# Performance work log

Hardware: AMD Instinct MI355X
Metric: run time of the kernel (lower is better)

## Reference

```python
import jax, jax.numpy as jnp
import numpy as np

D_MODEL = 1024

def setup_inputs() -> dict:
    key = jax.random.key(0)
    ks = jax.random.split(key, 7)
    s = 1.0 / np.sqrt(D_MODEL)
    x = jax.random.normal(ks[0], (4, 2048, D_MODEL), dtype=jnp.float32)
    wq_w = jax.random.uniform(ks[1], (D_MODEL, D_MODEL), jnp.float32, -s, s)
    wq_b = jax.random.uniform(ks[2], (D_MODEL,), jnp.float32, -s, s)
    wk_w = jax.random.uniform(ks[3], (D_MODEL, D_MODEL), jnp.float32, -s, s)
    wk_b = jax.random.uniform(ks[4], (D_MODEL,), jnp.float32, -s, s)
    wv_w = jax.random.uniform(ks[5], (D_MODEL, D_MODEL), jnp.float32, -s, s)
    wv_b = jax.random.uniform(ks[6], (D_MODEL,), jnp.float32, -s, s)
    return {"x": x, "wq_w": wq_w, "wq_b": wq_b, "wk_w": wk_w, "wk_b": wk_b, "wv_w": wv_w, "wv_b": wv_b}

def reference(x, wq_w, wq_b, wk_w, wk_b, wv_w, wv_b):
    # Linear: x @ W^T + b (torch nn.Linear convention)
    q = jnp.einsum('bsd,ed->bse', x, wq_w) + wq_b
    k = jnp.einsum('bsd,ed->bse', x, wk_w) + wk_b
    v = jnp.einsum('bsd,ed->bse', x, wv_w) + wv_b
    scale = 1.0 / jnp.sqrt(jnp.asarray(k.shape[-1], dtype=q.dtype))
    logits = jnp.einsum('bqd,bkd->bqk', q, k) * scale  # [B, S, S]
    attn = jax.nn.softmax(logits, axis=-1)
    out = jnp.einsum('bqk,bkd->bqd', attn, v)
    return (attn, out)
```

## Files before the change

kernel.cpp:

```cpp
#include <hip/hip_runtime.h>

typedef unsigned short u16;
typedef u16 u16x4 __attribute__((ext_vector_type(4)));
typedef u16 u16x8 __attribute__((ext_vector_type(8)));
typedef __bf16 bf16x8 __attribute__((ext_vector_type(8)));
typedef float f32x16 __attribute__((ext_vector_type(16)));

static __device__ __forceinline__ u16 f2bf(float f) {
  unsigned u = __builtin_bit_cast(unsigned, f);
  u += 0x7fffu + ((u >> 16) & 1u);
  return (u16)(u >> 16);
}
static __device__ __forceinline__ float bf2f(u16 h) {
  return __builtin_bit_cast(float, ((unsigned)h) << 16);
}

static __device__ __forceinline__ void gload_lds16(const u16* g, u16* l) {
  u16* gn = const_cast<u16*>(g);
  __builtin_amdgcn_global_load_lds(
      (__attribute__((address_space(1))) unsigned int*)gn,
      (__attribute__((address_space(3))) unsigned int*)l,
      16, 0, 0);
}

__global__ __launch_bounds__(256)
void cvt_f32_bf16(const float* __restrict__ in, u16* __restrict__ out) {
  const int i = blockIdx.x * 256 + threadIdx.x;
  float4 f = ((const float4*)in)[i];
  u16x4 o = { f2bf(f.x), f2bf(f.y), f2bf(f.z), f2bf(f.w) };
  ((u16x4*)out)[i] = o;
}

__global__ __launch_bounds__(256)
void cvt_w3(const float* __restrict__ a, const float* __restrict__ b,
            const float* __restrict__ c, u16* __restrict__ out) {
  const int blk = blockIdx.x;
  const int w = blk >> 10;
  const float* src = (w == 0) ? a : (w == 1) ? b : c;
  const int i = (blk & 1023) * 256 + threadIdx.x;
  float4 f = ((const float4*)src)[i];
  u16x4 o = { f2bf(f.x), f2bf(f.y), f2bf(f.z), f2bf(f.w) };
  ((u16x4*)(out + (size_t)w * 1048576ULL))[i] = o;
}

template<int MODE>
__global__ __launch_bounds__(256)
void gemm_bt(const u16* __restrict__ Ain, const u16* __restrict__ Bin,
             void* __restrict__ Cv,
             const float* __restrict__ b0, const float* __restrict__ b1,
             const float* __restrict__ b2,
             int lda, int ldb, int ldc, int K,
             unsigned long long sA, unsigned long long sB, unsigned long long sC,
             int nbx, int nby)
{
  constexpr int BM = 128, BN = 128, BK = 64;
  __shared__ alignas(16) u16 As[BM * BK];
  __shared__ alignas(16) u16 Bs[BN * BK];

  const int nbxy = nbx * nby;
  const int bid  = blockIdx.x;
  const int flat = (bid & 7) * ((int)gridDim.x >> 3) + (bid >> 3);
  const int z    = flat / nbxy;
  const int rr   = flat - z * nbxy;
  const int width = nbx << 3;
  const int gid  = rr / width;
  const int rw   = rr - gid * width;
  const int by   = (gid << 3) + (rw & 7);
  const int bx   = rw >> 3;

  const u16* A = Ain + z * sA;
  const u16* B = Bin + z * sB;

  const int tid  = threadIdx.x;
  const int wave = tid >> 6;
  const int lane = tid & 63;
  const int l32  = lane & 31;
  const int half = lane >> 5;
  const int wr   = wave >> 1;
  const int wc   = wave & 1;

  const int m0 = by * BM;
  const int n0 = bx * BN;

  const int lr = lane >> 3;
  const int sc = ((lane & 7) ^ lr) * 8;
  const u16* Ag = A + (size_t)(m0 + wave * 32 + lr) * lda + sc;
  const u16* Bg = B + (size_t)(n0 + wave * 32 + lr) * ldb + sc;
  u16* Asb = &As[(wave * 32) * BK];
  u16* Bsb = &Bs[(wave * 32) * BK];

  f32x16 acc[2][2];
  #pragma unroll
  for (int i = 0; i < 2; ++i)
    #pragma unroll
    for (int j = 0; j < 2; ++j)
      #pragma unroll
      for (int r = 0; r < 16; ++r)
        acc[i][j][r] = 0.f;

  for (int k0 = 0; k0 < K; k0 += BK) {
    gload_lds16(Ag + k0,                    Asb);
    gload_lds16(Ag + (size_t) 8 * lda + k0, Asb +  8 * BK);
    gload_lds16(Ag + (size_t)16 * lda + k0, Asb + 16 * BK);
    gload_lds16(Ag + (size_t)24 * lda + k0, Asb + 24 * BK);
    gload_lds16(Bg + k0,                    Bsb);
    gload_lds16(Bg + (size_t) 8 * ldb + k0, Bsb +  8 * BK);
    gload_lds16(Bg + (size_t)16 * ldb + k0, Bsb + 16 * BK);
    gload_lds16(Bg + (size_t)24 * ldb + k0, Bsb + 24 * BK);
    __syncthreads();

    #pragma unroll
    for (int ks = 0; ks < 4; ++ks) {
      bf16x8 af[2], bfr[2];
      #pragma unroll
      for (int ti = 0; ti < 2; ++ti) {
        const int row = wr * 64 + ti * 32 + l32;
        const int ch  = ((ks * 2 + half) ^ (row & 7)) * 8;
        af[ti] = *(const bf16x8*)&As[row * BK + ch];
      }
      #pragma unroll
      for (int tj = 0; tj < 2; ++tj) {
        const int row = wc * 64 + tj * 32 + l32;
        const int ch  = ((ks * 2 + half) ^ (row & 7)) * 8;
        bfr[tj] = *(const bf16x8*)&Bs[row * BK + ch];
      }
      #pragma unroll
      for (int ti = 0; ti < 2; ++ti)
        #pragma unroll
        for (int tj = 0; tj < 2; ++tj)
          acc[ti][tj] = __builtin_amdgcn_mfma_f32_32x32x16_bf16(af[ti], bfr[tj], acc[ti][tj], 0, 0, 0);
    }
    __syncthreads();
  }

  const int colb = n0 + wc * 64 + l32;
  const int rowb = m0 + wr * 64 + 4 * half;

  if constexpr (MODE == 0) {
    const int g = n0 >> 10;
    u16* Qb = (u16*)Cv;
    if (g < 2) {
      u16* Cb = Qb + (size_t)g * 8388608ULL;
      const float* bp = (g == 0) ? b0 : b1;
      const float qs = (g == 0) ? 0.03125f : 1.0f;
      #pragma unroll
      for (int tj = 0; tj < 2; ++tj) {
        const int col = (colb + tj * 32) & 1023;
        const float bv = bp[col];
        #pragma unroll
        for (int ti = 0; ti < 2; ++ti)
          #pragma unroll
          for (int g4 = 0; g4 < 4; ++g4)
            #pragma unroll
            for (int r = 0; r < 4; ++r) {
              const int row = rowb + ti * 32 + g4 * 8 + r;
              Cb[(size_t)row * 1024 + col] = f2bf((acc[ti][tj][g4 * 4 + r] + bv) * qs);
            }
      }
    } else {
      u16* Vt = Qb + 16777216ULL;
      #pragma unroll
      for (int tj = 0; tj < 2; ++tj) {
        const int col = (colb + tj * 32) & 1023;
        const float bv = b2[col];
        #pragma unroll
        for (int ti = 0; ti < 2; ++ti)
          #pragma unroll
          for (int g4 = 0; g4 < 4; ++g4) {
            const int row = rowb + ti * 32 + g4 * 8;
            u16x4 o;
            #pragma unroll
            for (int r = 0; r < 4; ++r) o[r] = f2bf(acc[ti][tj][g4 * 4 + r] + bv);
            const size_t idx = ((size_t)((row >> 11) * 1024 + col)) * 2048 + (row & 2047);
            *(u16x4*)&Vt[idx] = o;
          }
      }
    }
  } else if constexpr (MODE == 2) {
    u16* Cb = (u16*)Cv + z * sC;
    #pragma unroll
    for (int tj = 0; tj < 2; ++tj) {
      const int col = colb + tj * 32;
      #pragma unroll
      for (int ti = 0; ti < 2; ++ti)
        #pragma unroll
        for (int g4 = 0; g4 < 4; ++g4)
          #pragma unroll
          for (int r = 0; r < 4; ++r) {
            const int row = rowb + ti * 32 + g4 * 8 + r;
            Cb[(size_t)row * ldc + col] = f2bf(acc[ti][tj][g4 * 4 + r]);
          }
    }
  } else {
    float* Cf = (float*)Cv + z * sC;
    #pragma unroll
    for (int tj = 0; tj < 2; ++tj) {
      const int col = colb + tj * 32;
      #pragma unroll
      for (int ti = 0; ti < 2; ++ti)
        #pragma unroll
        for (int g4 = 0; g4 < 4; ++g4)
          #pragma unroll
          for (int r = 0; r < 4; ++r) {
            const int row = rowb + ti * 32 + g4 * 8 + r;
            Cf[(size_t)row * ldc + col] = acc[ti][tj][g4 * 4 + r];
          }
    }
  }
}

__global__ __launch_bounds__(256)
void softmax_rows(u16* __restrict__ logits, float* __restrict__ attn) {
  const int row = blockIdx.x;
  const int tid = threadIdx.x;
  u16*   lp = logits + (size_t)row * 2048 + tid * 8;
  float* ap = attn   + (size_t)row * 2048 + tid * 8;

  u16x8 raw = *(const u16x8*)lp;
  float v[8];
  #pragma unroll
  for (int j = 0; j < 8; ++j) v[j] = bf2f(raw[j]);

  float mx = v[0];
  #pragma unroll
  for (int j = 1; j < 8; ++j) mx = fmaxf(mx, v[j]);
  #pragma unroll
  for (int o = 32; o > 0; o >>= 1) mx = fmaxf(mx, __shfl_xor(mx, o, 64));

  __shared__ float smax[4], ssum[4];
  const int wv = tid >> 6, ln = tid & 63;
  if (ln == 0) smax[wv] = mx;
  __syncthreads();
  mx = fmaxf(fmaxf(smax[0], smax[1]), fmaxf(smax[2], smax[3]));

  float s = 0.f;
  #pragma unroll
  for (int j = 0; j < 8; ++j) { v[j] = __expf(v[j] - mx); s += v[j]; }
  #pragma unroll
  for (int o = 32; o > 0; o >>= 1) s += __shfl_xor(s, o, 64);
  if (ln == 0) ssum[wv] = s;
  __syncthreads();
  s = (ssum[0] + ssum[1]) + (ssum[2] + ssum[3]);
  const float inv = 1.f / s;

  u16x8 ob;
  #pragma unroll
  for (int j = 0; j < 8; ++j) { v[j] *= inv; ob[j] = f2bf(v[j]); }
  float4* apv = (float4*)ap;
  apv[0] = make_float4(v[0], v[1], v[2], v[3]);
  apv[1] = make_float4(v[4], v[5], v[6], v[7]);
  *(u16x8*)lp = ob;
}

extern "C" void kernel_launch(void* const* d_in, const int* in_sizes, int n_in,
                              void* d_out, int out_size, void* d_ws, size_t ws_size,
                              hipStream_t stream) {
  (void)in_sizes; (void)n_in; (void)out_size; (void)ws_size;
  const float* x    = (const float*)d_in[0];
  const float* wq_w = (const float*)d_in[1];
  const float* wq_b = (const float*)d_in[2];
  const float* wk_w = (const float*)d_in[3];
  const float* wk_b = (const float*)d_in[4];
  const float* wv_w = (const float*)d_in[5];
  const float* wv_b = (const float*)d_in[6];

  float* attn = (float*)d_out;
  float* outp = attn + 16777216ULL;

  u16* xb   = (u16*)d_ws;
  u16* wcat = xb   + 8388608ULL;
  u16* Qb   = wcat + 3145728ULL;
  u16* Kb   = Qb   + 8388608ULL;
  u16* Vt   = Kb   + 8388608ULL;
  u16* Lg   = Vt   + 8388608ULL;

  cvt_f32_bf16<<<8192, 256, 0, stream>>>(x, xb);
  cvt_w3<<<3072, 256, 0, stream>>>(wq_w, wk_w, wv_w, wcat);

  gemm_bt<0><<<1536, 256, 0, stream>>>(xb, wcat, Qb, wq_b, wk_b, wv_b,
                                       1024, 1024, 1024, 1024, 0, 0, 0, 24, 64);

  gemm_bt<2><<<1024, 256, 0, stream>>>(Qb, Kb, Lg, nullptr, nullptr, nullptr,
                                       1024, 1024, 2048, 1024,
                                       2097152ULL, 2097152ULL, 4194304ULL, 16, 16);

  softmax_rows<<<8192, 256, 0, stream>>>(Lg, attn);

  gemm_bt<3><<<512, 256, 0, stream>>>(Lg, Vt, outp, nullptr, nullptr, nullptr,
                                      2048, 2048, 1024, 2048,
                                      4194304ULL, 2097152ULL, 2097152ULL, 8, 16);
}
```

Baseline: 311.5 us.

## Add 256x256-tile 8-wave pipelined GEMM for QKV projection and QK^T

```diff
diff --git a/kernel.cpp b/kernel.cpp
--- a/kernel.cpp
+++ b/kernel.cpp
@@ -4,6 +4,7 @@
 typedef u16 u16x4 __attribute__((ext_vector_type(4)));
 typedef u16 u16x8 __attribute__((ext_vector_type(8)));
 typedef __bf16 bf16x8 __attribute__((ext_vector_type(8)));
+typedef float f32x4 __attribute__((ext_vector_type(4)));
 typedef float f32x16 __attribute__((ext_vector_type(16)));
 
 static __device__ __forceinline__ u16 f2bf(float f) {
@@ -41,6 +42,198 @@
   float4 f = ((const float4*)src)[i];
   u16x4 o = { f2bf(f.x), f2bf(f.y), f2bf(f.z), f2bf(f.w) };
   ((u16x4*)(out + (size_t)w * 1048576ULL))[i] = o;
+}
+
+
+#define MM16(a, b, c) __builtin_amdgcn_mfma_f32_16x16x32_bf16(a, b, c, 0, 0, 0)
+#define WAITV4 asm volatile("s_waitcnt vmcnt(4)" ::: "memory")
+#define WAITNONE (void)0
+
+#define STAGE_A(BUF, J, KT) \
+  gload_lds16(Ag + (size_t)(J) * 32 * lda + (KT), AsW + (BUF) * 16384 + (J) * 2048)
+#define STAGE_B(BUF, KS, RH, KT) \
+  gload_lds16(Bg + (size_t)(RH) * 32 * ldb + (KS) * 32 + (KT), \
+              BsW + (BUF) * 16384 + (KS) * 2048 + (RH) * 1024)
+
+#define APTR(BUF, MI, KS) \
+  ((const bf16x8*)(ArdBase + (BUF) * 16384 + (MI) * 1024 + ((pA0 ^ ((KS) << 2)) << 3)))
+#define BPTR(BUF, NI, KS) \
+  ((const bf16x8*)(BrdBase + (BUF) * 16384 + (KS) * 2048 + (NI) * 512))
+
+#define PHASE(BUF, MH, KS, WAITSTMT, ...) do {                              \
+    bf16x8 a0 = *APTR(BUF, (MH) * 4 + 0, KS);                               \
+    bf16x8 a1 = *APTR(BUF, (MH) * 4 + 1, KS);                               \
+    bf16x8 a2 = *APTR(BUF, (MH) * 4 + 2, KS);                               \
+    bf16x8 a3 = *APTR(BUF, (MH) * 4 + 3, KS);                               \
+    bf16x8 q0 = *BPTR(BUF, 0, KS);                                          \
+    bf16x8 q1 = *BPTR(BUF, 1, KS);                                          \
+    bf16x8 q2 = *BPTR(BUF, 2, KS);                                          \
+    bf16x8 q3 = *BPTR(BUF, 3, KS);                                          \
+    __VA_ARGS__;                                                            \
+    __builtin_amdgcn_sched_barrier(0);                                      \
+    __builtin_amdgcn_s_barrier();                                           \
+    __builtin_amdgcn_s_setprio(1);                                          \
+    acc[(MH)*4+0][0] = MM16(a0, q0, acc[(MH)*4+0][0]);                      \
+    acc[(MH)*4+1][0] = MM16(a1, q0, acc[(MH)*4+1][0]);                      \
+    acc[(MH)*4+2][0] = MM16(a2, q0, acc[(MH)*4+2][0]);                      \
+    acc[(MH)*4+3][0] = MM16(a3, q0, acc[(MH)*4+3][0]);                      \
+    acc[(MH)*4+0][1] = MM16(a0, q1, acc[(MH)*4+0][1]);                      \
+    acc[(MH)*4+1][1] = MM16(a1, q1, acc[(MH)*4+1][1]);                      \
+    acc[(MH)*4+2][1] = MM16(a2, q1, acc[(MH)*4+2][1]);                      \
+    acc[(MH)*4+3][1] = MM16(a3, q1, acc[(MH)*4+3][1]);                      \
+    acc[(MH)*4+0][2] = MM16(a0, q2, acc[(MH)*4+0][2]);                      \
+    acc[(MH)*4+1][2] = MM16(a1, q2, acc[(MH)*4+1][2]);                      \
+    acc[(MH)*4+2][2] = MM16(a2, q2, acc[(MH)*4+2][2]);                      \
+    acc[(MH)*4+3][2] = MM16(a3, q2, acc[(MH)*4+3][2]);                      \
+    acc[(MH)*4+0][3] = MM16(a0, q3, acc[(MH)*4+0][3]);                      \
+    acc[(MH)*4+1][3] = MM16(a1, q3, acc[(MH)*4+1][3]);                      \
+    acc[(MH)*4+2][3] = MM16(a2, q3, acc[(MH)*4+2][3]);                      \
+    acc[(MH)*4+3][3] = MM16(a3, q3, acc[(MH)*4+3][3]);                      \
+    __builtin_amdgcn_s_setprio(0);                                          \
+    WAITSTMT;                                                               \
+    __builtin_amdgcn_sched_barrier(0);                                      \
+    __builtin_amdgcn_s_barrier();                                           \
+  } while (0)
+
+template<int MODE>
+__global__ __launch_bounds__(512, 2)
+void gemm8p(const u16* __restrict__ Ain, const u16* __restrict__ Bin,
+            void* __restrict__ Cv,
+            const float* __restrict__ b0, const float* __restrict__ b1,
+            const float* __restrict__ b2,
+            int lda, int ldb, int ldc, int K,
+            unsigned long long sA, unsigned long long sB, unsigned long long sC,
+            int nbx, int nby)
+{
+  __shared__ alignas(16) u16 As[2 * 2 * 128 * 64];
+  __shared__ alignas(16) u16 Bs[2 * 4 * 2 * 64 * 32];
+
+  const int nbxy = nbx * nby;
+  const int bid  = blockIdx.x;
+  const int flat = (bid & 7) * ((int)gridDim.x >> 3) + (bid >> 3);
+  const int z    = flat / nbxy;
+  const int rr   = flat - z * nbxy;
+  const int width = nbx << 3;
+  const int gid  = rr / width;
+  const int rw   = rr - gid * width;
+  const int by   = (gid << 3) + (rw & 7);
+  const int bx   = rw >> 3;
+
+  const u16* A = Ain + z * sA;
+  const u16* B = Bin + z * sB;
+
+  const int tid  = threadIdx.x;
+  const int wave = tid >> 6;
+  const int lane = tid & 63;
+  const int wr   = wave >> 2;
+  const int wc   = wave & 3;
+  const int l16  = lane & 15;
+  const int l4   = lane >> 4;
+
+  const int m0 = by << 8;
+  const int n0 = bx << 8;
+
+  const int asr = wc * 8 + (lane >> 3);
+  const int asc = ((lane & 7) ^ (lane >> 3)) << 3;
+  const u16* Ag = A + (size_t)(m0 + wr * 128 + asr) * lda + asc;
+  u16* AsW = As + wr * 8192 + wc * 512;
+
+  const int bsr = wr * 16 + (lane >> 2);
+  const int bsc = ((lane & 3) ^ ((lane >> 3) & 3)) << 3;
+  const u16* Bg = B + (size_t)(n0 + wc * 64 + bsr) * ldb + bsc;
+  u16* BsW = Bs + wc * 4096 + wr * 512;
+
+  const u16* ArdBase = As + (wr * 128 + l16) * 64;
+  const int pA0 = l4 ^ (l16 & 7);
+  const u16* BrdBase = Bs + wc * 4096 + l16 * 32 + ((l4 ^ ((l16 >> 1) & 3)) << 3);
+
+  f32x4 acc[8][4];
+  #pragma unroll
+  for (int i = 0; i < 8; ++i)
+    #pragma unroll
+    for (int j = 0; j < 4; ++j)
+      #pragma unroll
+      for (int r = 0; r < 4; ++r)
+        acc[i][j][r] = 0.f;
+
+  STAGE_A(0, 0, 0); STAGE_A(0, 1, 0);
+  STAGE_B(0, 0, 0, 0); STAGE_B(0, 0, 1, 0);
+  STAGE_B(0, 1, 0, 0); STAGE_B(0, 1, 1, 0);
+  STAGE_A(0, 2, 0); STAGE_A(0, 3, 0);
+  WAITV4;
+  __builtin_amdgcn_sched_barrier(0);
+  __builtin_amdgcn_s_barrier();
+
+  const int NT = K >> 6;
+  for (int t = 0; t < NT; t += 2) {
+    {
+      const int kn = (t + 1) * 64;
+      PHASE(0, 0, 0, WAITV4,   STAGE_A(1, 0, kn); STAGE_A(1, 1, kn));
+      PHASE(0, 0, 1, WAITV4,   STAGE_B(1, 0, 0, kn); STAGE_B(1, 0, 1, kn));
+      PHASE(0, 1, 0, WAITNONE, STAGE_B(1, 1, 0, kn); STAGE_B(1, 1, 1, kn));
+      PHASE(0, 1, 1, WAITV4,   STAGE_A(1, 2, kn); STAGE_A(1, 3, kn));
+    }
+    {
+      const int kn = (t + 2 < NT) ? (t + 2) * 64 : 0;
+      PHASE(1, 0, 0, WAITV4,   STAGE_A(0, 0, kn); STAGE_A(0, 1, kn));
+      PHASE(1, 0, 1, WAITV4,   STAGE_B(0, 0, 0, kn); STAGE_B(0, 0, 1, kn));
+      PHASE(1, 1, 0, WAITNONE, STAGE_B(0, 1, 0, kn); STAGE_B(0, 1, 1, kn));
+      PHASE(1, 1, 1, WAITV4,   STAGE_A(0, 2, kn); STAGE_A(0, 3, kn));
+    }
+  }
+  asm volatile("s_waitcnt vmcnt(0)" ::: "memory");
+
+  if constexpr (MODE == 0) {
+    const int g = n0 >> 10;
+    const int colb = (n0 + wc * 64) & 1023;
+    const int rowb = m0 + wr * 128 + l4 * 4;
+    if (g < 2) {
+      u16* Cb = (u16*)Cv + (size_t)g * 8388608ULL;
+      const float* bp = (g == 0) ? b0 : b1;
+      const float qs = (g == 0) ? 0.03125f : 1.0f;
+      #pragma unroll
+      for (int ni = 0; ni < 4; ++ni) {
+        const int col = colb + ni * 16 + l16;
+        const float bv = bp[col];
+        #pragma unroll
+        for (int mi = 0; mi < 8; ++mi) {
+          const int row = rowb + mi * 16;
+          #pragma unroll
+          for (int r = 0; r < 4; ++r)
+            Cb[(size_t)(row + r) * 1024 + col] = f2bf((acc[mi][ni][r] + bv) * qs);
+        }
+      }
+    } else {
+      u16* Vt = (u16*)Cv + 16777216ULL;
+      #pragma unroll
+      for (int ni = 0; ni < 4; ++ni) {
+        const int col = colb + ni * 16 + l16;
+        const float bv = b2[col];
+        #pragma unroll
+        for (int mi = 0; mi < 8; ++mi) {
+          const int row = rowb + mi * 16;
+          u16x4 o;
+          #pragma unroll
+          for (int r = 0; r < 4; ++r) o[r] = f2bf(acc[mi][ni][r] + bv);
+          const size_t idx = ((size_t)((row >> 11) * 1024 + col)) * 2048 + (row & 2047);
+          *(u16x4*)&Vt[idx] = o;
+        }
+      }
+    }
+  } else {
+    u16* Cb = (u16*)Cv + (size_t)z * sC;
+    #pragma unroll
+    for (int ni = 0; ni < 4; ++ni) {
+      const int col = n0 + wc * 64 + ni * 16 + l16;
+      #pragma unroll
+      for (int mi = 0; mi < 8; ++mi) {
+        const int row = m0 + wr * 128 + mi * 16 + l4 * 4;
+        #pragma unroll
+        for (int r = 0; r < 4; ++r)
+          Cb[(size_t)(row + r) * ldc + col] = f2bf(acc[mi][ni][r]);
+      }
+    }
+  }
 }
 
 template<int MODE>
@@ -136,62 +329,7 @@
   const int colb = n0 + wc * 64 + l32;
   const int rowb = m0 + wr * 64 + 4 * half;
 
-  if constexpr (MODE == 0) {
-    const int g = n0 >> 10;
-    u16* Qb = (u16*)Cv;
-    if (g < 2) {
-      u16* Cb = Qb + (size_t)g * 8388608ULL;
-      const float* bp = (g == 0) ? b0 : b1;
-      const float qs = (g == 0) ? 0.03125f : 1.0f;
-      #pragma unroll
-      for (int tj = 0; tj < 2; ++tj) {
-        const int col = (colb + tj * 32) & 1023;
-        const float bv = bp[col];
-        #pragma unroll
-        for (int ti = 0; ti < 2; ++ti)
-          #pragma unroll
-          for (int g4 = 0; g4 < 4; ++g4)
-            #pragma unroll
-            for (int r = 0; r < 4; ++r) {
-              const int row = rowb + ti * 32 + g4 * 8 + r;
-              Cb[(size_t)row * 1024 + col] = f2bf((acc[ti][tj][g4 * 4 + r] + bv) * qs);
-            }
-      }
-    } else {
-      u16* Vt = Qb + 16777216ULL;
-      #pragma unroll
-      for (int tj = 0; tj < 2; ++tj) {
-        const int col = (colb + tj * 32) & 1023;
-        const float bv = b2[col];
-        #pragma unroll
-        for (int ti = 0; ti < 2; ++ti)
-          #pragma unroll
-          for (int g4 = 0; g4 < 4; ++g4) {
-            const int row = rowb + ti * 32 + g4 * 8;
-            u16x4 o;
-            #pragma unroll
-            for (int r = 0; r < 4; ++r) o[r] = f2bf(acc[ti][tj][g4 * 4 + r] + bv);
-            const size_t idx = ((size_t)((row >> 11) * 1024 + col)) * 2048 + (row & 2047);
-            *(u16x4*)&Vt[idx] = o;
-          }
-      }
-    }
-  } else if constexpr (MODE == 2) {
-    u16* Cb = (u16*)Cv + z * sC;
-    #pragma unroll
-    for (int tj = 0; tj < 2; ++tj) {
-      const int col = colb + tj * 32;
-      #pragma unroll
-      for (int ti = 0; ti < 2; ++ti)
-        #pragma unroll
-        for (int g4 = 0; g4 < 4; ++g4)
-          #pragma unroll
-          for (int r = 0; r < 4; ++r) {
-            const int row = rowb + ti * 32 + g4 * 8 + r;
-            Cb[(size_t)row * ldc + col] = f2bf(acc[ti][tj][g4 * 4 + r]);
-          }
-    }
-  } else {
+  if constexpr (MODE == 3) {
     float* Cf = (float*)Cv + z * sC;
     #pragma unroll
     for (int tj = 0; tj < 2; ++tj) {
@@ -277,12 +415,12 @@
   cvt_f32_bf16<<<8192, 256, 0, stream>>>(x, xb);
   cvt_w3<<<3072, 256, 0, stream>>>(wq_w, wk_w, wv_w, wcat);
 
-  gemm_bt<0><<<1536, 256, 0, stream>>>(xb, wcat, Qb, wq_b, wk_b, wv_b,
-                                       1024, 1024, 1024, 1024, 0, 0, 0, 24, 64);
-
-  gemm_bt<2><<<1024, 256, 0, stream>>>(Qb, Kb, Lg, nullptr, nullptr, nullptr,
-                                       1024, 1024, 2048, 1024,
-                                       2097152ULL, 2097152ULL, 4194304ULL, 16, 16);
+  gemm8p<0><<<384, 512, 0, stream>>>(xb, wcat, Qb, wq_b, wk_b, wv_b,
+                                     1024, 1024, 1024, 1024, 0, 0, 0, 12, 32);
+
+  gemm8p<2><<<256, 512, 0, stream>>>(Qb, Kb, Lg, nullptr, nullptr, nullptr,
+                                     1024, 1024, 2048, 1024,
+                                     2097152ULL, 2097152ULL, 4194304ULL, 8, 8);
 
   softmax_rows<<<8192, 256, 0, stream>>>(Lg, attn);
 
```

After: 326.4 us. 4.8% more time.

## Double-buffer GEMM LDS tiles with BK=32 and prefetch next tile

Applied to the files above, without the earlier changes.

```diff
diff --git a/kernel.cpp b/kernel.cpp
--- a/kernel.cpp
+++ b/kernel.cpp
@@ -53,9 +53,9 @@
              unsigned long long sA, unsigned long long sB, unsigned long long sC,
              int nbx, int nby)
 {
-  constexpr int BM = 128, BN = 128, BK = 64;
-  __shared__ alignas(16) u16 As[BM * BK];
-  __shared__ alignas(16) u16 Bs[BN * BK];
+  constexpr int BM = 128, BK = 32;
+  __shared__ alignas(16) u16 As[2 * BM * BK];
+  __shared__ alignas(16) u16 Bs[2 * BM * BK];
 
   const int nbxy = nbx * nby;
   const int bid  = blockIdx.x;
@@ -80,14 +80,15 @@
   const int wc   = wave & 1;
 
   const int m0 = by * BM;
-  const int n0 = bx * BN;
-
-  const int lr = lane >> 3;
-  const int sc = ((lane & 7) ^ lr) * 8;
-  const u16* Ag = A + (size_t)(m0 + wave * 32 + lr) * lda + sc;
-  const u16* Bg = B + (size_t)(n0 + wave * 32 + lr) * ldb + sc;
-  u16* Asb = &As[(wave * 32) * BK];
-  u16* Bsb = &Bs[(wave * 32) * BK];
+  const int n0 = bx * BM;
+
+  const int lr2 = lane >> 2;
+  const int pos = lane & 3;
+  const int gch = pos ^ ((lr2 >> 1) & 3);
+  const u16* Ag = A + (size_t)(m0 + wave * 16 + lr2) * lda + gch * 8;
+  const u16* Bg = B + (size_t)(n0 + wave * 16 + lr2) * ldb + gch * 8;
+  u16* Asb = &As[(wave * 16) * BK];
+  u16* Bsb = &Bs[(wave * 16) * BK];
 
   f32x16 acc[2][2];
   #pragma unroll
@@ -98,31 +99,37 @@
       for (int r = 0; r < 16; ++r)
         acc[i][j][r] = 0.f;
 
-  for (int k0 = 0; k0 < K; k0 += BK) {
-    gload_lds16(Ag + k0,                    Asb);
-    gload_lds16(Ag + (size_t) 8 * lda + k0, Asb +  8 * BK);
-    gload_lds16(Ag + (size_t)16 * lda + k0, Asb + 16 * BK);
-    gload_lds16(Ag + (size_t)24 * lda + k0, Asb + 24 * BK);
-    gload_lds16(Bg + k0,                    Bsb);
-    gload_lds16(Bg + (size_t) 8 * ldb + k0, Bsb +  8 * BK);
-    gload_lds16(Bg + (size_t)16 * ldb + k0, Bsb + 16 * BK);
-    gload_lds16(Bg + (size_t)24 * ldb + k0, Bsb + 24 * BK);
-    __syncthreads();
-
-    #pragma unroll
-    for (int ks = 0; ks < 4; ++ks) {
+  gload_lds16(Ag,                    Asb);
+  gload_lds16(Ag + (size_t)64 * lda, Asb + 2048);
+  gload_lds16(Bg,                    Bsb);
+  gload_lds16(Bg + (size_t)64 * ldb, Bsb + 2048);
+  __syncthreads();
+
+  const int NT = K >> 5;
+  for (int t = 0; t < NT; ++t) {
+    const int cur = (t & 1) * 4096;
+    const int nxt = cur ^ 4096;
+    const int kn  = (t + 1 < NT) ? (t + 1) * 32 : 0;
+
+    gload_lds16(Ag + kn,                    Asb + nxt);
+    gload_lds16(Ag + (size_t)64 * lda + kn, Asb + nxt + 2048);
+    gload_lds16(Bg + kn,                    Bsb + nxt);
+    gload_lds16(Bg + (size_t)64 * ldb + kn, Bsb + nxt + 2048);
+
+    #pragma unroll
+    for (int ks = 0; ks < 2; ++ks) {
       bf16x8 af[2], bfr[2];
       #pragma unroll
       for (int ti = 0; ti < 2; ++ti) {
         const int row = wr * 64 + ti * 32 + l32;
-        const int ch  = ((ks * 2 + half) ^ (row & 7)) * 8;
-        af[ti] = *(const bf16x8*)&As[row * BK + ch];
+        const int ch  = ((ks * 2 + half) ^ ((l32 >> 1) & 3)) * 8;
+        af[ti] = *(const bf16x8*)&As[cur + row * BK + ch];
       }
       #pragma unroll
       for (int tj = 0; tj < 2; ++tj) {
         const int row = wc * 64 + tj * 32 + l32;
-        const int ch  = ((ks * 2 + half) ^ (row & 7)) * 8;
-        bfr[tj] = *(const bf16x8*)&Bs[row * BK + ch];
+        const int ch  = ((ks * 2 + half) ^ ((l32 >> 1) & 3)) * 8;
+        bfr[tj] = *(const bf16x8*)&Bs[cur + row * BK + ch];
       }
       #pragma unroll
       for (int ti = 0; ti < 2; ++ti)
```

After: 334.9 us. +7.5%, slower.

## Enlarge GEMM block tile to 256x128 using 16x16x32 MFMA with new LDS swizzle

Applied to the files above, without the earlier changes.

```diff
diff --git a/kernel.cpp b/kernel.cpp
--- a/kernel.cpp
+++ b/kernel.cpp
@@ -4,7 +4,7 @@
 typedef u16 u16x4 __attribute__((ext_vector_type(4)));
 typedef u16 u16x8 __attribute__((ext_vector_type(8)));
 typedef __bf16 bf16x8 __attribute__((ext_vector_type(8)));
-typedef float f32x16 __attribute__((ext_vector_type(16)));
+typedef float f32x4 __attribute__((ext_vector_type(4)));
 
 static __device__ __forceinline__ u16 f2bf(float f) {
   unsigned u = __builtin_bit_cast(unsigned, f);
@@ -44,7 +44,7 @@
 }
 
 template<int MODE>
-__global__ __launch_bounds__(256)
+__global__ __launch_bounds__(256, 2)
 void gemm_bt(const u16* __restrict__ Ain, const u16* __restrict__ Bin,
              void* __restrict__ Cv,
              const float* __restrict__ b0, const float* __restrict__ b1,
@@ -53,9 +53,8 @@
              unsigned long long sA, unsigned long long sB, unsigned long long sC,
              int nbx, int nby)
 {
-  constexpr int BM = 128, BN = 128, BK = 64;
-  __shared__ alignas(16) u16 As[BM * BK];
-  __shared__ alignas(16) u16 Bs[BN * BK];
+  __shared__ alignas(16) u16 As[256 * 64];
+  __shared__ alignas(16) u16 Bs[2 * 128 * 32];
 
   const int nbxy = nbx * nby;
   const int bid  = blockIdx.x;
@@ -74,137 +73,126 @@
   const int tid  = threadIdx.x;
   const int wave = tid >> 6;
   const int lane = tid & 63;
-  const int l32  = lane & 31;
-  const int half = lane >> 5;
+  const int l16  = lane & 15;
+  const int l4   = (lane >> 4) & 3;
   const int wr   = wave >> 1;
   const int wc   = wave & 1;
 
-  const int m0 = by * BM;
-  const int n0 = bx * BN;
-
-  const int lr = lane >> 3;
-  const int sc = ((lane & 7) ^ lr) * 8;
-  const u16* Ag = A + (size_t)(m0 + wave * 32 + lr) * lda + sc;
-  const u16* Bg = B + (size_t)(n0 + wave * 32 + lr) * ldb + sc;
-  u16* Asb = &As[(wave * 32) * BK];
-  u16* Bsb = &Bs[(wave * 32) * BK];
-
-  f32x16 acc[2][2];
-  #pragma unroll
-  for (int i = 0; i < 2; ++i)
-    #pragma unroll
-    for (int j = 0; j < 2; ++j)
-      #pragma unroll
-      for (int r = 0; r < 16; ++r)
+  const int m0 = by << 8;
+  const int n0 = bx << 7;
+
+  const u16* Ag = A + (size_t)(m0 + wave * 64 + (lane >> 3)) * lda
+                    + (((lane & 7) ^ (lane >> 3)) << 3);
+  u16* Asb = &As[wave * 64 * 64];
+  const u16* Bg = B + (size_t)(n0 + wave * 32 + (lane >> 2)) * ldb
+                    + (((lane & 3) ^ ((lane >> 3) & 3)) << 3);
+  u16* Bsb = &Bs[wave * 32 * 32];
+
+  const int pA = l4 ^ (l16 & 7);
+  const u16* ArdBase = As + (size_t)(wr * 128 + l16) * 64;
+  const u16* BrdBase = Bs + (size_t)(wc * 64 + l16) * 32
+                          + ((l4 ^ ((l16 >> 1) & 3)) << 3);
+
+  f32x4 acc[8][4];
+  #pragma unroll
+  for (int i = 0; i < 8; ++i)
+    #pragma unroll
+    for (int j = 0; j < 4; ++j)
+      #pragma unroll
+      for (int r = 0; r < 4; ++r)
         acc[i][j][r] = 0.f;
 
-  for (int k0 = 0; k0 < K; k0 += BK) {
-    gload_lds16(Ag + k0,                    Asb);
-    gload_lds16(Ag + (size_t) 8 * lda + k0, Asb +  8 * BK);
-    gload_lds16(Ag + (size_t)16 * lda + k0, Asb + 16 * BK);
-    gload_lds16(Ag + (size_t)24 * lda + k0, Asb + 24 * BK);
-    gload_lds16(Bg + k0,                    Bsb);
-    gload_lds16(Bg + (size_t) 8 * ldb + k0, Bsb +  8 * BK);
-    gload_lds16(Bg + (size_t)16 * ldb + k0, Bsb + 16 * BK);
-    gload_lds16(Bg + (size_t)24 * ldb + k0, Bsb + 24 * BK);
+  for (int k0 = 0; k0 < K; k0 += 64) {
+    #pragma unroll
+    for (int j = 0; j < 8; ++j)
+      gload_lds16(Ag + (size_t)(j * 8) * lda + k0, Asb + j * 512);
+    gload_lds16(Bg + k0,                          Bsb);
+    gload_lds16(Bg + (size_t)16 * ldb + k0,       Bsb + 512);
+    gload_lds16(Bg + k0 + 32,                     Bsb + 4096);
+    gload_lds16(Bg + (size_t)16 * ldb + k0 + 32,  Bsb + 4096 + 512);
     __syncthreads();
 
     #pragma unroll
-    for (int ks = 0; ks < 4; ++ks) {
-      bf16x8 af[2], bfr[2];
-      #pragma unroll
-      for (int ti = 0; ti < 2; ++ti) {
-        const int row = wr * 64 + ti * 32 + l32;
-        const int ch  = ((ks * 2 + half) ^ (row & 7)) * 8;
-        af[ti] = *(const bf16x8*)&As[row * BK + ch];
-      }
-      #pragma unroll
-      for (int tj = 0; tj < 2; ++tj) {
-        const int row = wc * 64 + tj * 32 + l32;
-        const int ch  = ((ks * 2 + half) ^ (row & 7)) * 8;
-        bfr[tj] = *(const bf16x8*)&Bs[row * BK + ch];
-      }
-      #pragma unroll
-      for (int ti = 0; ti < 2; ++ti)
-        #pragma unroll
-        for (int tj = 0; tj < 2; ++tj)
-          acc[ti][tj] = __builtin_amdgcn_mfma_f32_32x32x16_bf16(af[ti], bfr[tj], acc[ti][tj], 0, 0, 0);
+    for (int ks = 0; ks < 2; ++ks) {
+      bf16x8 af[8], bf[4];
+      #pragma unroll
+      for (int mi = 0; mi < 8; ++mi)
+        af[mi] = *(const bf16x8*)(ArdBase + mi * 1024 + ((pA ^ (ks << 2)) << 3));
+      #pragma unroll
+      for (int ni = 0; ni < 4; ++ni)
+        bf[ni] = *(const bf16x8*)(BrdBase + ks * 4096 + ni * 512);
+      #pragma unroll
+      for (int mi = 0; mi < 8; ++mi)
+        #pragma unroll
+        for (int ni = 0; ni < 4; ++ni)
+          acc[mi][ni] = __builtin_amdgcn_mfma_f32_16x16x32_bf16(af[mi], bf[ni], acc[mi][ni], 0, 0, 0);
     }
     __syncthreads();
   }
 
-  const int colb = n0 + wc * 64 + l32;
-  const int rowb = m0 + wr * 64 + 4 * half;
+  const int colq = wc * 64;
+  const int rowb = m0 + wr * 128 + l4 * 4;
 
   if constexpr (MODE == 0) {
     const int g = n0 >> 10;
-    u16* Qb = (u16*)Cv;
     if (g < 2) {
-      u16* Cb = Qb + (size_t)g * 8388608ULL;
+      u16* Cb = (u16*)Cv + (size_t)g * 8388608ULL;
       const float* bp = (g == 0) ? b0 : b1;
       const float qs = (g == 0) ? 0.03125f : 1.0f;
       #pragma unroll
-      for (int tj = 0; tj < 2; ++tj) {
-        const int col = (colb + tj * 32) & 1023;
+      for (int ni = 0; ni < 4; ++ni) {
+        const int col = (n0 + colq + ni * 16 + l16) & 1023;
         const float bv = bp[col];
         #pragma unroll
-        for (int ti = 0; ti < 2; ++ti)
+        for (int mi = 0; mi < 8; ++mi) {
+          const int row = rowb + mi * 16;
           #pragma unroll
-          for (int g4 = 0; g4 < 4; ++g4)
-            #pragma unroll
-            for (int r = 0; r < 4; ++r) {
-              const int row = rowb + ti * 32 + g4 * 8 + r;
-              Cb[(size_t)row * 1024 + col] = f2bf((acc[ti][tj][g4 * 4 + r] + bv) * qs);
-            }
+          for (int r = 0; r < 4; ++r)
+            Cb[(size_t)(row + r) * 1024 + col] = f2bf((acc[mi][ni][r] + bv) * qs);
+        }
       }
     } else {
-      u16* Vt = Qb + 16777216ULL;
-      #pragma unroll
-      for (int tj = 0; tj < 2; ++tj) {
-        const int col = (colb + tj * 32) & 1023;
+      u16* Vt = (u16*)Cv + 16777216ULL;
+      #pragma unroll
+      for (int ni = 0; ni < 4; ++ni) {
+        const int col = (n0 + colq + ni * 16 + l16) & 1023;
         const float bv = b2[col];
         #pragma unroll
-        for (int ti = 0; ti < 2; ++ti)
+        for (int mi = 0; mi < 8; ++mi) {
+          const int row = rowb + mi * 16;
+          u16x4 o;
           #pragma unroll
-          for (int g4 = 0; g4 < 4; ++g4) {
-            const int row = rowb + ti * 32 + g4 * 8;
-            u16x4 o;
-            #pragma unroll
-            for (int r = 0; r < 4; ++r) o[r] = f2bf(acc[ti][tj][g4 * 4 + r] + bv);
-            const size_t idx = ((size_t)((row >> 11) * 1024 + col)) * 2048 + (row & 2047);
-            *(u16x4*)&Vt[idx] = o;
-          }
+          for (int r = 0; r < 4; ++r) o[r] = f2bf(acc[mi][ni][r] + bv);
+          const size_t idx = ((size_t)((row >> 11) * 1024 + col)) * 2048 + (row & 2047);
+          *(u16x4*)&Vt[idx] = o;
+        }
       }
     }
   } else if constexpr (MODE == 2) {
-    u16* Cb = (u16*)Cv + z * sC;
-    #pragma unroll
-    for (int tj = 0; tj < 2; ++tj) {
-      const int col = colb + tj * 32;
-      #pragma unroll
-      for (int ti = 0; ti < 2; ++ti)
-        #pragma unroll
-        for (int g4 = 0; g4 < 4; ++g4)
-          #pragma unroll
-          for (int r = 0; r < 4; ++r) {
-            const int row = rowb + ti * 32 + g4 * 8 + r;
-            Cb[(size_t)row * ldc + col] = f2bf(acc[ti][tj][g4 * 4 + r]);
-          }
+    u16* Cb = (u16*)Cv + (size_t)z * sC;
+    #pragma unroll
+    for (int ni = 0; ni < 4; ++ni) {
+      const int col = n0 + colq + ni * 16 + l16;
+      #pragma unroll
+      for (int mi = 0; mi < 8; ++mi) {
+        const int row = rowb + mi * 16;
+        #pragma unroll
+        for (int r = 0; r < 4; ++r)
+          Cb[(size_t)(row + r) * ldc + col] = f2bf(acc[mi][ni][r]);
+      }
     }
   } else {
-    float* Cf = (float*)Cv + z * sC;
-    #pragma unroll
-    for (int tj = 0; tj < 2; ++tj) {
-      const int col = colb + tj * 32;
-      #pragma unroll
-      for (int ti = 0; ti < 2; ++ti)
-        #pragma unroll
-        for (int g4 = 0; g4 < 4; ++g4)
-          #pragma unroll
-          for (int r = 0; r < 4; ++r) {
-            const int row = rowb + ti * 32 + g4 * 8 + r;
-            Cf[(size_t)row * ldc + col] = acc[ti][tj][g4 * 4 + r];
-          }
+    float* Cf = (float*)Cv + (size_t)z * sC;
+    #pragma unroll
+    for (int ni = 0; ni < 4; ++ni) {
+      const int col = n0 + colq + ni * 16 + l16;
+      #pragma unroll
+      for (int mi = 0; mi < 8; ++mi) {
+        const int row = rowb + mi * 16;
+        #pragma unroll
+        for (int r = 0; r < 4; ++r)
+          Cf[(size_t)(row + r) * ldc + col] = acc[mi][ni][r];
+      }
     }
   }
 }
@@ -277,16 +265,16 @@
   cvt_f32_bf16<<<8192, 256, 0, stream>>>(x, xb);
   cvt_w3<<<3072, 256, 0, stream>>>(wq_w, wk_w, wv_w, wcat);
 
-  gemm_bt<0><<<1536, 256, 0, stream>>>(xb, wcat, Qb, wq_b, wk_b, wv_b,
-                                       1024, 1024, 1024, 1024, 0, 0, 0, 24, 64);
-
-  gemm_bt<2><<<1024, 256, 0, stream>>>(Qb, Kb, Lg, nullptr, nullptr, nullptr,
-                                       1024, 1024, 2048, 1024,
-                                       2097152ULL, 2097152ULL, 4194304ULL, 16, 16);
+  gemm_bt<0><<<768, 256, 0, stream>>>(xb, wcat, Qb, wq_b, wk_b, wv_b,
+                                      1024, 1024, 1024, 1024, 0, 0, 0, 24, 32);
+
+  gemm_bt<2><<<512, 256, 0, stream>>>(Qb, Kb, Lg, nullptr, nullptr, nullptr,
+                                      1024, 1024, 2048, 1024,
+                                      2097152ULL, 2097152ULL, 4194304ULL, 16, 8);
 
   softmax_rows<<<8192, 256, 0, stream>>>(Lg, attn);
 
-  gemm_bt<3><<<512, 256, 0, stream>>>(Lg, Vt, outp, nullptr, nullptr, nullptr,
+  gemm_bt<3><<<256, 256, 0, stream>>>(Lg, Vt, outp, nullptr, nullptr, nullptr,
                                       2048, 2048, 1024, 2048,
-                                      4194304ULL, 2097152ULL, 2097152ULL, 8, 16);
-}
+                                      4194304ULL, 2097152ULL, 2097152ULL, 8, 8);
+}
```

New measurement: 320.5 us. 1.03x slower.
